# Performance work log

Hardware: AMD Instinct MI355X
Metric: run time of the kernel (lower is better)

## Reference

```python
import jax, jax.numpy as jnp
import numpy as np
from jax import lax

B, C_IN, C_OUT, H, W, E = 16, 256, 256, 32, 32, 8


def setup_inputs() -> dict:
    key = jax.random.key(0)
    k = jax.random.split(key, 5)
    x = jax.random.normal(k[0], (B, C_IN, H, W), dtype=jnp.float32)
    # router: Conv2d(C_IN, E, kernel_size=1) -> weight [E, C_IN], bias [E]
    wc = jax.random.normal(k[1], (E, C_IN), dtype=jnp.float32) / np.sqrt(C_IN)
    bc = jnp.zeros((E,), dtype=jnp.float32)
    # experts: E x Conv2d(C_IN, C_OUT, 3, padding=1) + ReLU
    we = jax.random.normal(k[2], (E, C_OUT, C_IN, 3, 3), dtype=jnp.float32) / np.sqrt(C_IN * 9)
    be = jnp.zeros((E, C_OUT), dtype=jnp.float32)
    return {"x": x, "wc": wc, "bc": bc, "we": we, "be": be}


def reference(x, wc, bc, we, be):
    Bx = x.shape[0]
    # controller: 1x1 conv then global avg-pool == pool then linear
    pooled = jnp.mean(x, axis=(2, 3))                      # [B, C_IN]
    logits = pooled @ wc.T + bc                            # [B, E]
    decisions = jnp.argmax(logits, axis=1)                 # [B] int
    # run ALL experts on the full batch as one grouped conv: weight [E*C_OUT, C_IN, 3, 3]
    w_all = we.reshape(E * C_OUT, C_IN, 3, 3)
    y = lax.conv_general_dilated(
        x, w_all, window_strides=(1, 1), padding="SAME",
        dimension_numbers=("NCHW", "OIHW", "NCHW"))        # [B, E*C_OUT, H, W]
    y = y + be.reshape(1, E * C_OUT, 1, 1)
    y = jax.nn.relu(y).reshape(Bx, E, C_OUT, H, W)
    # faithful to forward_test: out block i is components[dec[i]](x) for the FULL batch
    # out[i*B + j] = y[j, dec[i]]
    gathered = y[:, decisions]                             # [j, i, C_OUT, H, W]
    out = jnp.swapaxes(gathered, 0, 1).reshape(Bx * Bx, C_OUT, H, W)
    return out
```

## Files before the change

kernel.cpp:

```cpp
#include <hip/hip_runtime.h>
#include <hip/hip_bf16.h>
#include <stdint.h>

#define B_    16
#define CIN   256
#define COUT  256
#define E_    8
#define HW    1024
#define PH    34
#define PW    34

typedef __attribute__((ext_vector_type(8))) short  short8;
typedef __attribute__((ext_vector_type(4))) float  floatx4;

#define XT_OFF 17408
#define XT_BYTES (B_*PH*PW*CIN*2)
#define WT_OFF (XT_OFF + XT_BYTES)

__device__ __forceinline__ void gld_lds16(const void* g, void* l) {
    __builtin_amdgcn_global_load_lds(
        (const __attribute__((address_space(1))) unsigned int*)g,
        (__attribute__((address_space(3))) unsigned int*)l,
        16, 0, 0);
}

__global__ void pool_kernel(const float* __restrict__ x, float* __restrict__ pooled) {
    int b = blockIdx.x, c = blockIdx.y;
    const float4* p = (const float4*)(x + ((size_t)b*CIN + c)*HW);
    int t = threadIdx.x;
    float4 v = p[t];
    float s = v.x + v.y + v.z + v.w;
    #pragma unroll
    for (int o = 32; o > 0; o >>= 1) s += __shfl_down(s, o, 64);
    __shared__ float wsum[4];
    if ((t & 63) == 0) wsum[t >> 6] = s;
    __syncthreads();
    if (t == 0) pooled[b*CIN + c] = (wsum[0]+wsum[1]+wsum[2]+wsum[3]) * (1.0f/1024.0f);
}

__global__ void decide_kernel(const float* __restrict__ pooled, const float* __restrict__ wc,
                              const float* __restrict__ bc, int* __restrict__ dec) {
    int t = threadIdx.x;
    int b = t >> 3, e = t & 7;
    float acc = bc[e];
    const float4* pp = (const float4*)(pooled + b*CIN);
    const float4* ww = (const float4*)(wc + e*CIN);
    #pragma unroll 4
    for (int i = 0; i < CIN/4; ++i) {
        float4 p = pp[i], w = ww[i];
        acc += p.x*w.x + p.y*w.y + p.z*w.z + p.w*w.w;
    }
    __shared__ float lg[16][8];
    lg[b][e] = acc;
    __syncthreads();
    if (e == 0) {
        float best = lg[b][0]; int bi = 0;
        #pragma unroll
        for (int j = 1; j < 8; ++j) { if (lg[b][j] > best) { best = lg[b][j]; bi = j; } }
        dec[b] = bi;
    }
}

__global__ void xpose_kernel(const float* __restrict__ x, unsigned short* __restrict__ xt) {
    int b = blockIdx.x;
    int hw0 = blockIdx.y * 32;
    int ci0 = blockIdx.z * 32;
    __shared__ float tile[32][33];
    int t = threadIdx.x;
    int j = t & 31;
    int i = t >> 5;
    #pragma unroll
    for (int p = 0; p < 4; ++p)
        tile[i + p*8][j] = x[((size_t)b*CIN + ci0 + i + p*8)*HW + hw0 + j];
    __syncthreads();
    int cw = t & 31;
    int rw = t >> 5;
    #pragma unroll
    for (int p = 0; p < 4; ++p) {
        int hw = hw0 + rw + p*8;
        int h = hw >> 5, w = hw & 31;
        __hip_bfloat16 hv = __float2bfloat16(tile[cw][rw + p*8]);
        xt[(((size_t)b*PH + h + 1)*PW + (w + 1))*CIN + ci0 + cw] = *(unsigned short*)&hv;
    }
}

__global__ void wpose_kernel(const float* __restrict__ we, unsigned short* __restrict__ wt) {
    int e = blockIdx.x >> 8, co = blockIdx.x & 255;
    __shared__ float buf[CIN*9];
    const float* src = we + ((size_t)e*COUT + co)*CIN*9;
    int t = threadIdx.x;
    #pragma unroll
    for (int k = 0; k < 9; ++k) buf[t + k*256] = src[t + k*256];
    __syncthreads();
    #pragma unroll
    for (int rs = 0; rs < 9; ++rs) {
        __hip_bfloat16 h = __float2bfloat16(buf[t*9 + rs]);
        wt[(((size_t)e*9 + rs)*COUT + co)*CIN + t] = *(unsigned short*)&h;
    }
}

__global__ __launch_bounds__(256) void conv_kernel(
    const unsigned short* __restrict__ xt, const unsigned short* __restrict__ wt,
    const float* __restrict__ be, const int* __restrict__ dec,
    float* __restrict__ out) {

    int tile = blockIdx.x;
    int b = blockIdx.y;
    int e = blockIdx.z;
    int mt = tile >> 3, nt = tile & 7;

    int dcs[16];
    #pragma unroll
    for (int i = 0; i < 16; ++i) dcs[i] = dec[i];
    bool active = false;
    #pragma unroll
    for (int i = 0; i < 16; ++i) active |= (dcs[i] == e);
    if (!active) return;

    __shared__ __align__(16) unsigned short sA[2][512*8];
    __shared__ __align__(16) unsigned short sB[2][1024*8];

    int t = threadIdx.x;
    int wave = t >> 6, lane = t & 63;
    int wm = wave >> 1, wn = wave & 1;
    int kg = lane >> 4, ln = lane & 15;

    int ph0 = nt * 4;
    int co0 = mt * 128;

    floatx4 acc[4][4];
    #pragma unroll
    for (int i = 0; i < 4; ++i)
        #pragma unroll
        for (int j = 0; j < 4; ++j) acc[i][j] = (floatx4)0.0f;

    const unsigned short* xb = xt + ((size_t)b*PH + ph0)*PW*CIN;
    const unsigned short* wb = wt + (size_t)e*9*COUT*CIN + (size_t)co0*CIN;

    auto stageA = [&](int ck, int sh, int buf) {
        const unsigned short* wsrc = wb + (size_t)sh*COUT*CIN + ck*32;
        #pragma unroll
        for (int k = 0; k < 2; ++k) {
            int c = t + k*256;
            int row = c >> 2, gs = c & 3;
            int g = gs ^ ((row >> 1) & 3);
            gld_lds16(wsrc + (size_t)row*CIN + g*8, &sA[buf][c*8]);
        }
    };
    auto stageB = [&](int ck, int buf) {
        const unsigned short* xsrc = xb + ck*32;
        #pragma unroll
        for (int k = 0; k < 3; ++k) {
            int c = t + k*256;
            int rB = c >> 2, gs = c & 3;
            int g = gs ^ ((rB >> 1) & 3);
            gld_lds16(xsrc + (size_t)rB*CIN + g*8, &sB[buf][c*8]);
        }
        if (t < 64) {
            int c = t + 768;
            int cc = c < 816 ? c : 815;
            int rB = cc >> 2, gs = cc & 3;
            int g = gs ^ ((rB >> 1) & 3);
            gld_lds16(xsrc + (size_t)rB*CIN + g*8, &sB[buf][c*8]);
        }
    };

    stageB(0, 0);
    stageA(0, 0, 0);
    __syncthreads();

    for (int ck = 0; ck < 8; ++ck) {
        for (int sh = 0; sh < 9; ++sh) {
            int it = ck*9 + sh;
            int ab = it & 1, bb_ = ck & 1;

            if (sh < 8) {
                stageA(ck, sh + 1, ab ^ 1);
            } else if (ck < 7) {
                stageA(ck + 1, 0, ab ^ 1);
                stageB(ck + 1, bb_ ^ 1);
            }

            short8 a[4], bv[4];
            #pragma unroll
            for (int im = 0; im < 4; ++im) {
                int row = wm*64 + im*16 + ln;
                int cL = row*4 + (kg ^ ((row >> 1) & 3));
                a[im] = *(const short8*)(&sA[ab][cL*8]);
            }
            int r = sh / 3, s = sh - r*3;
            #pragma unroll
            for (int in = 0; in < 4; ++in) {
                int n  = wn*64 + in*16 + ln;
                int hl = n >> 5, wl = n & 31;
                int rB = (hl + r)*34 + (wl + s);
                int cL = rB*4 + (kg ^ ((rB >> 1) & 3));
                bv[in] = *(const short8*)(&sB[bb_][cL*8]);
            }

            #pragma unroll
            for (int im = 0; im < 4; ++im)
                #pragma unroll
                for (int in = 0; in < 4; ++in)
                    acc[im][in] = __builtin_amdgcn_mfma_f32_16x16x32_bf16(a[im], bv[in], acc[im][in], 0, 0, 0);

            __syncthreads();
        }
    }

    #pragma unroll
    for (int im = 0; im < 4; ++im) {
        int co = co0 + wm*64 + im*16 + kg*4;
        #pragma unroll
        for (int rg = 0; rg < 4; ++rg) {
            float bvv = be[e*COUT + co + rg];
            #pragma unroll
            for (int in = 0; in < 4; ++in) {
                float v = acc[im][in][rg] + bvv;
                acc[im][in][rg] = v > 0.0f ? v : 0.0f;
            }
        }
    }
    for (int i = 0; i < 16; ++i) {
        if (dcs[i] != e) continue;
        float* ob = out + (size_t)(i*16 + b)*COUT*HW;
        #pragma unroll
        for (int im = 0; im < 4; ++im) {
            int co = co0 + wm*64 + im*16 + kg*4;
            #pragma unroll
            for (int in = 0; in < 4; ++in) {
                int hw = nt*128 + wn*64 + in*16 + ln;
                #pragma unroll
                for (int rg = 0; rg < 4; ++rg)
                    ob[(size_t)(co + rg)*HW + hw] = acc[im][in][rg];
            }
        }
    }
}

extern "C" void kernel_launch(void* const* d_in, const int* in_sizes, int n_in,
                              void* d_out, int out_size, void* d_ws, size_t ws_size,
                              hipStream_t stream) {
    const float* x  = (const float*)d_in[0];
    const float* wc = (const float*)d_in[1];
    const float* bc = (const float*)d_in[2];
    const float* we = (const float*)d_in[3];
    const float* be = (const float*)d_in[4];
    float* out = (float*)d_out;

    char* ws = (char*)d_ws;
    int*   dec    = (int*)ws;
    float* pooled = (float*)(ws + 64);
    unsigned short* xt = (unsigned short*)(ws + XT_OFF);
    unsigned short* wt = (unsigned short*)(ws + WT_OFF);

    hipMemsetAsync(xt, 0, XT_BYTES, stream);

    pool_kernel  <<<dim3(16, 256), 256, 0, stream>>>(x, pooled);
    decide_kernel<<<1, 128, 0, stream>>>(pooled, wc, bc, dec);
    xpose_kernel <<<dim3(16, 32, 8), 256, 0, stream>>>(x, xt);
    wpose_kernel <<<2048, 256, 0, stream>>>(we, wt);
    conv_kernel  <<<dim3(16, 16, 8), 256, 0, stream>>>(xt, wt, be, dec, out);
}
```

Baseline: 459.9 us.

## Triple-buffer weight tiles with vmcnt waits, swap MFMA operands for vector stores

The conv kernel moves from double to triple buffering of the weight tiles, prefetching two shifts ahead. It replaces __syncthreads with explicit s_waitcnt vmcnt counts plus s_barrier so loads stay in flight across iterations. MFMA operands are swapped so each lane holds four consecutive output pixels, which turns the epilogue writes of the very large output into 16-byte vector stores. The transpose kernels also pack eight bf16 values per 16-byte store; the hand-counted vmcnt values risk races if the load counts per wave are wrong.

```diff
diff --git a/kernel.cpp b/kernel.cpp
--- a/kernel.cpp
+++ b/kernel.cpp
@@ -73,14 +73,18 @@
     for (int p = 0; p < 4; ++p)
         tile[i + p*8][j] = x[((size_t)b*CIN + ci0 + i + p*8)*HW + hw0 + j];
     __syncthreads();
-    int cw = t & 31;
-    int rw = t >> 5;
-    #pragma unroll
-    for (int p = 0; p < 4; ++p) {
-        int hw = hw0 + rw + p*8;
+    if (t < 128) {
+        int g = t & 3;
+        int hwl = t >> 2;
+        int hw = hw0 + hwl;
         int h = hw >> 5, w = hw & 31;
-        __hip_bfloat16 hv = __float2bfloat16(tile[cw][rw + p*8]);
-        xt[(((size_t)b*PH + h + 1)*PW + (w + 1))*CIN + ci0 + cw] = *(unsigned short*)&hv;
+        short8 v;
+        #pragma unroll
+        for (int q = 0; q < 8; ++q) {
+            __hip_bfloat16 hv = __float2bfloat16(tile[g*8 + q][hwl]);
+            v[q] = *(short*)&hv;
+        }
+        *(short8*)&xt[(((size_t)b*PH + h + 1)*PW + (w + 1))*CIN + ci0 + g*8] = v;
     }
 }
 
@@ -92,10 +96,15 @@
     #pragma unroll
     for (int k = 0; k < 9; ++k) buf[t + k*256] = src[t + k*256];
     __syncthreads();
-    #pragma unroll
-    for (int rs = 0; rs < 9; ++rs) {
-        __hip_bfloat16 h = __float2bfloat16(buf[t*9 + rs]);
-        wt[(((size_t)e*9 + rs)*COUT + co)*CIN + t] = *(unsigned short*)&h;
+    for (int idx = t; idx < 288; idx += 256) {
+        int rs = idx >> 5, grp = idx & 31;
+        short8 v;
+        #pragma unroll
+        for (int q = 0; q < 8; ++q) {
+            __hip_bfloat16 h = __float2bfloat16(buf[(grp*8 + q)*9 + rs]);
+            v[q] = *(short*)&h;
+        }
+        *(short8*)&wt[(((size_t)e*9 + rs)*COUT + co)*CIN + grp*8] = v;
     }
 }
 
@@ -117,8 +126,8 @@
     for (int i = 0; i < 16; ++i) active |= (dcs[i] == e);
     if (!active) return;
 
-    __shared__ __align__(16) unsigned short sA[2][512*8];
-    __shared__ __align__(16) unsigned short sB[2][1024*8];
+    __shared__ __align__(16) unsigned short sA[3][512*8];
+    __shared__ __align__(16) unsigned short sB[2][832*8];
 
     int t = threadIdx.x;
     int wave = t >> 6, lane = t & 63;
@@ -167,19 +176,24 @@
 
     stageB(0, 0);
     stageA(0, 0, 0);
-    __syncthreads();
+    stageA(0, 1, 1);
+    asm volatile("s_waitcnt vmcnt(2)" ::: "memory");
+    __builtin_amdgcn_s_barrier();
 
     for (int ck = 0; ck < 8; ++ck) {
+        int bb_ = ck & 1;
         for (int sh = 0; sh < 9; ++sh) {
             int it = ck*9 + sh;
-            int ab = it & 1, bb_ = ck & 1;
-
-            if (sh < 8) {
-                stageA(ck, sh + 1, ab ^ 1);
-            } else if (ck < 7) {
-                stageA(ck + 1, 0, ab ^ 1);
-                stageB(ck + 1, bb_ ^ 1);
-            }
+            int ab = it % 3;
+
+            int nit = it + 2;
+            bool doA = (nit < 72);
+            if (doA) {
+                int nck = nit / 9;
+                stageA(nck, nit - nck*9, nit % 3);
+            }
+            bool doB = (sh == 7) && (ck < 7);
+            if (doB) stageB(ck + 1, bb_ ^ 1);
 
             short8 a[4], bv[4];
             #pragma unroll
@@ -202,38 +216,46 @@
             for (int im = 0; im < 4; ++im)
                 #pragma unroll
                 for (int in = 0; in < 4; ++in)
-                    acc[im][in] = __builtin_amdgcn_mfma_f32_16x16x32_bf16(a[im], bv[in], acc[im][in], 0, 0, 0);
-
-            __syncthreads();
-        }
-    }
-
-    #pragma unroll
-    for (int im = 0; im < 4; ++im) {
-        int co = co0 + wm*64 + im*16 + kg*4;
-        #pragma unroll
-        for (int rg = 0; rg < 4; ++rg) {
-            float bvv = be[e*COUT + co + rg];
-            #pragma unroll
-            for (int in = 0; in < 4; ++in) {
-                float v = acc[im][in][rg] + bvv;
+                    acc[im][in] = __builtin_amdgcn_mfma_f32_16x16x32_bf16(bv[in], a[im], acc[im][in], 0, 0, 0);
+
+            if (doA) {
+                if (doB) {
+                    if (wave == 0) asm volatile("s_waitcnt vmcnt(6) lgkmcnt(0)" ::: "memory");
+                    else           asm volatile("s_waitcnt vmcnt(5) lgkmcnt(0)" ::: "memory");
+                } else {
+                    asm volatile("s_waitcnt vmcnt(2) lgkmcnt(0)" ::: "memory");
+                }
+            } else {
+                asm volatile("s_waitcnt vmcnt(0) lgkmcnt(0)" ::: "memory");
+            }
+            __builtin_amdgcn_s_barrier();
+        }
+    }
+
+    float bias[4];
+    #pragma unroll
+    for (int im = 0; im < 4; ++im)
+        bias[im] = be[e*COUT + co0 + wm*64 + im*16 + ln];
+    #pragma unroll
+    for (int im = 0; im < 4; ++im)
+        #pragma unroll
+        for (int in = 0; in < 4; ++in)
+            #pragma unroll
+            for (int rg = 0; rg < 4; ++rg) {
+                float v = acc[im][in][rg] + bias[im];
                 acc[im][in][rg] = v > 0.0f ? v : 0.0f;
             }
-        }
-    }
+
     for (int i = 0; i < 16; ++i) {
         if (dcs[i] != e) continue;
         float* ob = out + (size_t)(i*16 + b)*COUT*HW;
         #pragma unroll
         for (int im = 0; im < 4; ++im) {
-            int co = co0 + wm*64 + im*16 + kg*4;
-            #pragma unroll
-            for (int in = 0; in < 4; ++in) {
-                int hw = nt*128 + wn*64 + in*16 + ln;
-                #pragma unroll
-                for (int rg = 0; rg < 4; ++rg)
-                    ob[(size_t)(co + rg)*HW + hw] = acc[im][in][rg];
-            }
+            int co = co0 + wm*64 + im*16 + ln;
+            float* orow = ob + (size_t)co*HW + nt*128 + wn*64 + kg*4;
+            #pragma unroll
+            for (int in = 0; in < 4; ++in)
+                *(floatx4*)(orow + in*16) = acc[im][in];
         }
     }
 }
```

New measurement: 453.6 us. No clear change (-1.4%).
